# Performance work log

Hardware: AMD Instinct MI355X
Metric: run time of the kernel (lower is better)

## Reference

```python
import jax, jax.numpy as jnp
import numpy as np

N_NODES = 100000
N_EDGES = 1600000
DIM = 64
LN_EPS = 1e-5


def setup_inputs() -> dict:
    key = jax.random.key(0)
    ks = jax.random.split(key, 8)
    x = jax.random.normal(ks[0], (N_NODES, DIM), dtype=jnp.float32)
    edge_row = jax.random.randint(ks[1], (N_EDGES,), 0, N_NODES, dtype=jnp.int32)
    edge_col = jax.random.randint(ks[2], (N_EDGES,), 0, N_NODES, dtype=jnp.int32)
    edge_val = jax.random.uniform(ks[3], (N_EDGES,), dtype=jnp.float32)
    W = jax.random.normal(ks[4], (DIM, DIM), dtype=jnp.float32) * (1.0 / np.sqrt(DIM))
    b = jax.random.normal(ks[5], (DIM,), dtype=jnp.float32) * 0.01
    gamma = jnp.ones((DIM,), dtype=jnp.float32)
    beta = jnp.zeros((DIM,), dtype=jnp.float32)
    return {"x": x, "edge_row": edge_row, "edge_col": edge_col,
            "edge_val": edge_val, "W": W, "b": b, "gamma": gamma, "beta": beta}


def reference(x, edge_row, edge_col, edge_val, W, b, gamma, beta):
    # SpMM: out[r] += val * x[c] for each edge (r, c, val)  (= torch.sparse.mm(adj, x))
    msgs = edge_val[:, None] * x[edge_col]                      # [E, D]
    agg = jax.ops.segment_sum(msgs, edge_row, num_segments=x.shape[0])  # [N, D]
    # Linear
    h = agg @ W.T + b                                           # [N, D]
    # LayerNorm over last dim
    mu = jnp.mean(h, axis=-1, keepdims=True)
    var = jnp.mean(jnp.square(h - mu), axis=-1, keepdims=True)
    h = (h - mu) * jax.lax.rsqrt(var + LN_EPS) * gamma + beta
    # ReLU (dropout p=0.0 -> identity)
    return jax.nn.relu(h)
```

## Files before the change

### kernel.cpp

```cpp
#include <hip/hip_runtime.h>
#include <hip/hip_fp16.h>

#define DIM 64
#define RPB 128
#define NSCAT 512
#define MAXBUK 1024
#define ECAP 2432
#define CAP 384

typedef _Float16 half8_t __attribute__((ext_vector_type(8)));
typedef float f32x4_t __attribute__((ext_vector_type(4)));

__device__ __forceinline__ float readlane_f(float v, int l) {
  return __uint_as_float(__builtin_amdgcn_readlane(__float_as_uint(v), l));
}

__global__ __launch_bounds__(256) void scatter_kernel(
    const float* __restrict__ x, const int* __restrict__ erow,
    const int* __restrict__ ecol, const float* __restrict__ eval,
    float* __restrict__ agg, int E) {
  int t = blockIdx.x * 256 + threadIdx.x;
  int e = t >> 4;
  if (e >= E) return;
  int lid = t & 15;
  int r = erow[e];
  int c = ecol[e];
  float v = eval[e];
  const float4 xv =
      *reinterpret_cast<const float4*>(x + (size_t)c * DIM + lid * 4);
  float* dst = agg + (size_t)r * DIM + lid * 4;
  atomicAdd(dst + 0, v * xv.x);
  atomicAdd(dst + 1, v * xv.y);
  atomicAdd(dst + 2, v * xv.z);
  atomicAdd(dst + 3, v * xv.w);
}

__global__ __launch_bounds__(256) void fused_linear_ln_relu(
    const float* __restrict__ agg, const float* __restrict__ W,
    const float* __restrict__ bias, const float* __restrict__ gamma,
    const float* __restrict__ beta, float* __restrict__ out, int N) {
  __shared__ float Wt[64 * 65];
  for (int i = threadIdx.x; i < 64 * 64; i += 256) {
    int d = i >> 6, k = i & 63;
    Wt[k * 65 + d] = W[i];
  }
  __syncthreads();

  const int wave = threadIdx.x >> 6;
  const int lane = threadIdx.x & 63;
  const int node0 = blockIdx.x * 16 + wave * 4;

  float a0 = 0.f, a1 = 0.f, a2 = 0.f, a3 = 0.f;
  if (node0 + 0 < N) a0 = agg[(size_t)(node0 + 0) * DIM + lane];
  if (node0 + 1 < N) a1 = agg[(size_t)(node0 + 1) * DIM + lane];
  if (node0 + 2 < N) a2 = agg[(size_t)(node0 + 2) * DIM + lane];
  if (node0 + 3 < N) a3 = agg[(size_t)(node0 + 3) * DIM + lane];

  float acc0 = 0.f, acc1 = 0.f, acc2 = 0.f, acc3 = 0.f;
#pragma unroll
  for (int k = 0; k < 64; ++k) {
    float w = Wt[k * 65 + lane];
    acc0 = fmaf(readlane_f(a0, k), w, acc0);
    acc1 = fmaf(readlane_f(a1, k), w, acc1);
    acc2 = fmaf(readlane_f(a2, k), w, acc2);
    acc3 = fmaf(readlane_f(a3, k), w, acc3);
  }

  const float bv = bias[lane];
  const float gv = gamma[lane];
  const float btv = beta[lane];
  float accs[4] = {acc0, acc1, acc2, acc3};
#pragma unroll
  for (int j = 0; j < 4; ++j) {
    int node = node0 + j;
    if (node >= N) continue;
    float h = accs[j] + bv;
    float s1 = h, s2 = h * h;
#pragma unroll
    for (int off = 32; off; off >>= 1) {
      s1 += __shfl_xor(s1, off, 64);
      s2 += __shfl_xor(s2, off, 64);
    }
    float mu = s1 * (1.0f / 64.0f);
    float var = s2 * (1.0f / 64.0f) - mu * mu;
    float inv = rsqrtf(var + 1e-5f);
    float y = (h - mu) * inv * gv + btv;
    out[(size_t)node * DIM + lane] = fmaxf(y, 0.0f);
  }
}

__global__ __launch_bounds__(256) void scatter_reserve_and_cvt(
    const int* __restrict__ erow, const int* __restrict__ ecol,
    const float* __restrict__ eval, int* __restrict__ gcnt,
    uint2* __restrict__ binned, int E, int cpb, int NB,
    const float* __restrict__ x, __half* __restrict__ xh, int n4) {
  if (blockIdx.x >= NSCAT) {
    int i = (blockIdx.x - NSCAT) * 256 + threadIdx.x;
    if (i < n4) {
      float4 f = reinterpret_cast<const float4*>(x)[i];
      __half2 a = __floats2half2_rn(f.x, f.y);
      __half2 b = __floats2half2_rn(f.z, f.w);
      uint2 o;
      o.x = *reinterpret_cast<unsigned*>(&a);
      o.y = *reinterpret_cast<unsigned*>(&b);
      reinterpret_cast<uint2*>(xh)[i] = o;
    }
    return;
  }

  __shared__ int cnt_l[MAXBUK];
  __shared__ int cur_l[MAXBUK];

  const int tid = threadIdx.x;
  const int xcd = blockIdx.x & 7;
  const int base = blockIdx.x * cpb;
  const int end = min(E, base + cpb);

  for (int i = tid; i < NB; i += 256) cnt_l[i] = 0;
  __syncthreads();
  for (int e = base + tid; e < end; e += 256)
    atomicAdd(&cnt_l[erow[e] >> 7], 1);
  __syncthreads();
  for (int i = tid; i < NB; i += 256) {
    int c = cnt_l[i];
    cur_l[i] = c ? atomicAdd(&gcnt[xcd * NB + i], c) : 0;
  }
  __syncthreads();
  for (int e = base + tid; e < end; e += 256) {
    int r = erow[e];
    int b = r >> 7;
    uint2 p;
    p.x = ((unsigned)ecol[e] << 7) | (unsigned)(r & 127);
    p.y = __float_as_uint(eval[e]);
    int pos = atomicAdd(&cur_l[b], 1);
    if (pos < CAP)
      binned[(size_t)(xcd * NB + b) * CAP + pos] = p;
  }
}

template <typename XT>
__global__ __launch_bounds__(512) void fused_sort_gather_mfma_ln(
    const XT* __restrict__ xg, const uint2* __restrict__ binned,
    const int* __restrict__ gcnt, const float* __restrict__ W,
    const float* __restrict__ bias, const float* __restrict__ gamma,
    const float* __restrict__ beta, float* __restrict__ out, int N, int NB) {
  __shared__ uint2 ebuf[ECAP];
  __shared__ _Float16 A_lds[8][16 * 72];
  __shared__ int hist[RPB];
  __shared__ int rs_l[RPB + 1];
  __shared__ int cur[RPB];
  __shared__ int wsum2[2];

  const int tid = threadIdx.x;
  const int b = blockIdx.x;

  const int wave = tid >> 6;
  const int lane = tid & 63;
  const int gw = (tid >> 4) & 3;
  const int lid = tid & 15;

  if (tid < RPB) hist[tid] = 0;
  __syncthreads();
#pragma unroll 1
  for (int xcd = 0; xcd < 8; ++xcd) {
    const uint2* seg = binned + (size_t)(xcd * NB + b) * CAP;
    const int sc = min(gcnt[xcd * NB + b], CAP);
    for (int e = tid; e < sc; e += 512) atomicAdd(&hist[seg[e].x & 127], 1);
  }
  __syncthreads();
  {
    int v = (tid < RPB) ? hist[tid] : 0;
    int ps = v;
#pragma unroll
    for (int off = 1; off < 64; off <<= 1) {
      int nn = __shfl_up(ps, off, 64);
      if ((tid & 63) >= off) ps += nn;
    }
    if (tid == 63) wsum2[0] = ps;
    if (tid == 127) wsum2[1] = ps;
    __syncthreads();
    if (tid < RPB) {
      int ex = ps - v + (tid >= 64 ? wsum2[0] : 0);
      rs_l[tid] = min(ex, ECAP);
      cur[tid] = ex;
    }
    if (tid == 0) rs_l[RPB] = min(wsum2[0] + wsum2[1], ECAP);
    __syncthreads();
  }
#pragma unroll 1
  for (int xcd = 0; xcd < 8; ++xcd) {
    const uint2* seg = binned + (size_t)(xcd * NB + b) * CAP;
    const int sc = min(gcnt[xcd * NB + b], CAP);
    for (int e = tid; e < sc; e += 512) {
      uint2 p = seg[e];
      int pos = atomicAdd(&cur[p.x & 127], 1);
      if (pos < ECAP) ebuf[pos] = p;
    }
  }
  __syncthreads();

#pragma unroll 1
  for (int m = 0; m < 4; ++m) {
    const int lr = gw * 4 + m;
    const int rl = wave * 16 + lr;
    const int sl = rs_l[rl];
    const int el = max(rs_l[rl + 1], sl);
    float4 acc = make_float4(0.f, 0.f, 0.f, 0.f);
#pragma unroll 1
    for (int j = sl; j < el; j += 8) {
      uint2 p[8];
#pragma unroll
      for (int i = 0; i < 8; ++i) {
        int idx = j + i;
        idx = idx < el ? idx : el - 1;
        p[i] = ebuf[idx];
      }
      if constexpr (sizeof(XT) == 2) {
        uint2 xv[8];
#pragma unroll
        for (int i = 0; i < 8; ++i)
          xv[i] = *reinterpret_cast<const uint2*>(
              xg + (size_t)(p[i].x >> 7) * DIM + lid * 4);
#pragma unroll
        for (int i = 0; i < 8; ++i) {
          float v = (j + i < el) ? __uint_as_float(p[i].y) : 0.0f;
          float2 f01 = __half22float2(*reinterpret_cast<__half2*>(&xv[i].x));
          float2 f23 = __half22float2(*reinterpret_cast<__half2*>(&xv[i].y));
          acc.x = fmaf(v, f01.x, acc.x);
          acc.y = fmaf(v, f01.y, acc.y);
          acc.z = fmaf(v, f23.x, acc.z);
          acc.w = fmaf(v, f23.y, acc.w);
        }
      } else {
        float4 xv[8];
#pragma unroll
        for (int i = 0; i < 8; ++i)
          xv[i] = *reinterpret_cast<const float4*>(
              (const float*)xg + (size_t)(p[i].x >> 7) * DIM + lid * 4);
#pragma unroll
        for (int i = 0; i < 8; ++i) {
          float v = (j + i < el) ? __uint_as_float(p[i].y) : 0.0f;
          acc.x = fmaf(v, xv[i].x, acc.x);
          acc.y = fmaf(v, xv[i].y, acc.y);
          acc.z = fmaf(v, xv[i].z, acc.z);
          acc.w = fmaf(v, xv[i].w, acc.w);
        }
      }
    }
    __half2 lo = __floats2half2_rn(acc.x, acc.y);
    __half2 hi = __floats2half2_rn(acc.z, acc.w);
    uint2 pk;
    pk.x = *reinterpret_cast<unsigned*>(&lo);
    pk.y = *reinterpret_cast<unsigned*>(&hi);
    *reinterpret_cast<uint2*>(&A_lds[wave][lr * 72 + lid * 4]) = pk;
  }

  asm volatile("s_waitcnt lgkmcnt(0)" ::: "memory");
  __builtin_amdgcn_sched_barrier(0);

  const int dcol = lane & 15;
  const int kg = lane >> 4;

  half8_t bf[4][2];
#pragma unroll
  for (int t = 0; t < 4; ++t)
#pragma unroll
    for (int hh = 0; hh < 2; ++hh) {
      const float* wr = W + (dcol + 16 * t) * 64 + kg * 8 + 32 * hh;
      float4 w0 = *reinterpret_cast<const float4*>(wr);
      float4 w1 = *reinterpret_cast<const float4*>(wr + 4);
      half8_t hf;
      hf[0] = (_Float16)w0.x; hf[1] = (_Float16)w0.y;
      hf[2] = (_Float16)w0.z; hf[3] = (_Float16)w0.w;
      hf[4] = (_Float16)w1.x; hf[5] = (_Float16)w1.y;
      hf[6] = (_Float16)w1.z; hf[7] = (_Float16)w1.w;
      bf[t][hh] = hf;
    }

  half8_t af0 =
      *reinterpret_cast<const half8_t*>(&A_lds[wave][dcol * 72 + kg * 8]);
  half8_t af1 =
      *reinterpret_cast<const half8_t*>(&A_lds[wave][dcol * 72 + kg * 8 + 32]);

  f32x4_t dacc[4];
#pragma unroll
  for (int t = 0; t < 4; ++t) {
    f32x4_t z = {0.f, 0.f, 0.f, 0.f};
    z = __builtin_amdgcn_mfma_f32_16x16x32_f16(af0, bf[t][0], z, 0, 0, 0);
    z = __builtin_amdgcn_mfma_f32_16x16x32_f16(af1, bf[t][1], z, 0, 0, 0);
    dacc[t] = z;
  }

  const int q = lane >> 4;
  float bv[4], gv[4], btv[4];
#pragma unroll
  for (int t = 0; t < 4; ++t) {
    int d = dcol + 16 * t;
    bv[t] = bias[d];
    gv[t] = gamma[d];
    btv[t] = beta[d];
  }

#pragma unroll
  for (int j = 0; j < 4; ++j) {
    const int node = b * RPB + wave * 16 + q * 4 + j;
    float h0 = dacc[0][j] + bv[0];
    float h1 = dacc[1][j] + bv[1];
    float h2 = dacc[2][j] + bv[2];
    float h3 = dacc[3][j] + bv[3];
    float s1 = h0 + h1 + h2 + h3;
    float s2 = fmaf(h0, h0, fmaf(h1, h1, fmaf(h2, h2, h3 * h3)));
#pragma unroll
    for (int off = 1; off < 16; off <<= 1) {
      s1 += __shfl_xor(s1, off, 16);
      s2 += __shfl_xor(s2, off, 16);
    }
    float mu = s1 * (1.0f / 64.0f);
    float var = s2 * (1.0f / 64.0f) - mu * mu;
    float inv = rsqrtf(var + 1e-5f);
    if (node < N) {
      float* o = out + (size_t)node * DIM + dcol;
      o[0]  = fmaxf((h0 - mu) * inv * gv[0] + btv[0], 0.f);
      o[16] = fmaxf((h1 - mu) * inv * gv[1] + btv[1], 0.f);
      o[32] = fmaxf((h2 - mu) * inv * gv[2] + btv[2], 0.f);
      o[48] = fmaxf((h3 - mu) * inv * gv[3] + btv[3], 0.f);
    }
  }
}

extern "C" void kernel_launch(void* const* d_in, const int* in_sizes, int n_in,
                              void* d_out, int out_size, void* d_ws,
                              size_t ws_size, hipStream_t stream) {
  const float* x = (const float*)d_in[0];
  const int* erow = (const int*)d_in[1];
  const int* ecol = (const int*)d_in[2];
  const float* eval = (const float*)d_in[3];
  const float* W = (const float*)d_in[4];
  const float* bias = (const float*)d_in[5];
  const float* gamma = (const float*)d_in[6];
  const float* beta = (const float*)d_in[7];
  float* out = (float*)d_out;

  const int N = in_sizes[0] / DIM;
  const int E = in_sizes[1];

  const int NB = (N + RPB - 1) / RPB;
  const int cpb = (E + NSCAT - 1) / NSCAT;

  size_t gcnt_bytes = (size_t)8 * NB * sizeof(int);
  size_t binned_off = (gcnt_bytes + 15) & ~(size_t)15;
  size_t need_base = binned_off + (size_t)8 * NB * CAP * sizeof(uint2);
  size_t xh_off = (need_base + 15) & ~(size_t)15;
  size_t need_fp16 = xh_off + (size_t)N * DIM * sizeof(__half);

  if (ws_size >= need_base && NB <= MAXBUK) {
    int* gcnt = (int*)d_ws;
    uint2* binned = (uint2*)((char*)d_ws + binned_off);
    const bool use_fp16 = (ws_size >= need_fp16);
    __half* xh = (__half*)((char*)d_ws + xh_off);

    hipMemsetAsync(gcnt, 0, gcnt_bytes, stream);

    const int n4 = use_fp16 ? (N * DIM / 4) : 0;
    const int cvt_blocks = use_fp16 ? (n4 + 255) / 256 : 0;
    scatter_reserve_and_cvt<<<NSCAT + cvt_blocks, 256, 0, stream>>>(
        erow, ecol, eval, gcnt, binned, E, cpb, NB, x, xh, n4);
    if (use_fp16) {
      fused_sort_gather_mfma_ln<__half><<<NB, 512, 0, stream>>>(
          xh, binned, gcnt, W, bias, gamma, beta, out, N, NB);
    } else {
      fused_sort_gather_mfma_ln<float><<<NB, 512, 0, stream>>>(
          x, binned, gcnt, W, bias, gamma, beta, out, N, NB);
    }
  } else {
    const size_t agg_bytes = (size_t)N * DIM * sizeof(float);
    float* agg = (ws_size >= agg_bytes) ? (float*)d_ws : out;
    hipMemsetAsync(agg, 0, agg_bytes, stream);
    long long total = (long long)E * 16;
    int blocks = (int)((total + 255) / 256);
    scatter_kernel<<<blocks, 256, 0, stream>>>(x, erow, ecol, eval, agg, E);
    fused_linear_ln_relu<<<(N + 15) / 16, 256, 0, stream>>>(agg, W, bias,
                                                            gamma, beta, out, N);
  }
}
```

Before: 98.66 us.

## Cache binned edges in registers and widen fp16 gather to 16-byte loads

The binned-edge segments are now read once into registers (one entry per thread per XCD segment), used for both the histogram and the scatter passes, instead of being reloaded from global memory. The column index is pre-shifted when stored into LDS, so the gather loop no longer shifts it. For the fp16 path, each lane now loads 8 halves (16 bytes) per edge with 8 lanes per row and two rows per lane group, replacing 4-half loads with 16 lanes per row. This halves the number of load instructions and doubles the per-lane accumulator work. The register caching assumes each segment holds at most 512 entries, which holds because CAP is 384.

```diff
diff --git a/kernel.cpp b/kernel.cpp
--- a/kernel.cpp
+++ b/kernel.cpp
@@ -156,16 +156,22 @@
 
   const int wave = tid >> 6;
   const int lane = tid & 63;
-  const int gw = (tid >> 4) & 3;
-  const int lid = tid & 15;
-
+
+  uint2 myp[8];
+  bool myok[8];
   if (tid < RPB) hist[tid] = 0;
   __syncthreads();
-#pragma unroll 1
+#pragma unroll
   for (int xcd = 0; xcd < 8; ++xcd) {
     const uint2* seg = binned + (size_t)(xcd * NB + b) * CAP;
     const int sc = min(gcnt[xcd * NB + b], CAP);
-    for (int e = tid; e < sc; e += 512) atomicAdd(&hist[seg[e].x & 127], 1);
+    bool ok = tid < sc;
+    myok[xcd] = ok;
+    myp[xcd].x = 0; myp[xcd].y = 0;
+    if (ok) {
+      myp[xcd] = seg[tid];
+      atomicAdd(&hist[myp[xcd].x & 127], 1);
+    }
   }
   __syncthreads();
   {
@@ -187,56 +193,97 @@
     if (tid == 0) rs_l[RPB] = min(wsum2[0] + wsum2[1], ECAP);
     __syncthreads();
   }
+#pragma unroll
+  for (int xcd = 0; xcd < 8; ++xcd) {
+    if (myok[xcd]) {
+      uint2 p = myp[xcd];
+      int pos = atomicAdd(&cur[p.x & 127], 1);
+      if (pos < ECAP) {
+        uint2 q;
+        q.x = p.x >> 7;
+        q.y = p.y;
+        ebuf[pos] = q;
+      }
+    }
+  }
+  __syncthreads();
+
+  if constexpr (sizeof(XT) == 2) {
+    const int g8 = lane >> 3;
+    const int l8 = lane & 7;
 #pragma unroll 1
-  for (int xcd = 0; xcd < 8; ++xcd) {
-    const uint2* seg = binned + (size_t)(xcd * NB + b) * CAP;
-    const int sc = min(gcnt[xcd * NB + b], CAP);
-    for (int e = tid; e < sc; e += 512) {
-      uint2 p = seg[e];
-      int pos = atomicAdd(&cur[p.x & 127], 1);
-      if (pos < ECAP) ebuf[pos] = p;
-    }
-  }
-  __syncthreads();
-
+    for (int m = 0; m < 2; ++m) {
+      const int lr = g8 * 2 + m;
+      const int rl = wave * 16 + lr;
+      const int sl = rs_l[rl];
+      const int el = max(rs_l[rl + 1], sl);
+      float a[8] = {0.f, 0.f, 0.f, 0.f, 0.f, 0.f, 0.f, 0.f};
 #pragma unroll 1
-  for (int m = 0; m < 4; ++m) {
-    const int lr = gw * 4 + m;
-    const int rl = wave * 16 + lr;
-    const int sl = rs_l[rl];
-    const int el = max(rs_l[rl + 1], sl);
-    float4 acc = make_float4(0.f, 0.f, 0.f, 0.f);
-#pragma unroll 1
-    for (int j = sl; j < el; j += 8) {
-      uint2 p[8];
-#pragma unroll
-      for (int i = 0; i < 8; ++i) {
-        int idx = j + i;
-        idx = idx < el ? idx : el - 1;
-        p[i] = ebuf[idx];
-      }
-      if constexpr (sizeof(XT) == 2) {
-        uint2 xv[8];
+      for (int j = sl; j < el; j += 8) {
+        uint2 p[8];
+#pragma unroll
+        for (int i = 0; i < 8; ++i) {
+          int idx = j + i;
+          idx = idx < el ? idx : el - 1;
+          p[i] = ebuf[idx];
+        }
+        uint4 xv[8];
 #pragma unroll
         for (int i = 0; i < 8; ++i)
-          xv[i] = *reinterpret_cast<const uint2*>(
-              xg + (size_t)(p[i].x >> 7) * DIM + lid * 4);
+          xv[i] = *reinterpret_cast<const uint4*>(
+              xg + (size_t)p[i].x * DIM + l8 * 8);
 #pragma unroll
         for (int i = 0; i < 8; ++i) {
           float v = (j + i < el) ? __uint_as_float(p[i].y) : 0.0f;
-          float2 f01 = __half22float2(*reinterpret_cast<__half2*>(&xv[i].x));
-          float2 f23 = __half22float2(*reinterpret_cast<__half2*>(&xv[i].y));
-          acc.x = fmaf(v, f01.x, acc.x);
-          acc.y = fmaf(v, f01.y, acc.y);
-          acc.z = fmaf(v, f23.x, acc.z);
-          acc.w = fmaf(v, f23.y, acc.w);
+          float2 f0 = __half22float2(*reinterpret_cast<__half2*>(&xv[i].x));
+          float2 f1 = __half22float2(*reinterpret_cast<__half2*>(&xv[i].y));
+          float2 f2 = __half22float2(*reinterpret_cast<__half2*>(&xv[i].z));
+          float2 f3 = __half22float2(*reinterpret_cast<__half2*>(&xv[i].w));
+          a[0] = fmaf(v, f0.x, a[0]);
+          a[1] = fmaf(v, f0.y, a[1]);
+          a[2] = fmaf(v, f1.x, a[2]);
+          a[3] = fmaf(v, f1.y, a[3]);
+          a[4] = fmaf(v, f2.x, a[4]);
+          a[5] = fmaf(v, f2.y, a[5]);
+          a[6] = fmaf(v, f3.x, a[6]);
+          a[7] = fmaf(v, f3.y, a[7]);
         }
-      } else {
+      }
+      __half2 h0 = __floats2half2_rn(a[0], a[1]);
+      __half2 h1 = __floats2half2_rn(a[2], a[3]);
+      __half2 h2 = __floats2half2_rn(a[4], a[5]);
+      __half2 h3 = __floats2half2_rn(a[6], a[7]);
+      uint4 pk;
+      pk.x = *reinterpret_cast<unsigned*>(&h0);
+      pk.y = *reinterpret_cast<unsigned*>(&h1);
+      pk.z = *reinterpret_cast<unsigned*>(&h2);
+      pk.w = *reinterpret_cast<unsigned*>(&h3);
+      *reinterpret_cast<uint4*>(&A_lds[wave][lr * 72 + l8 * 8]) = pk;
+    }
+  } else {
+    const int gw = (tid >> 4) & 3;
+    const int lid = tid & 15;
+#pragma unroll 1
+    for (int m = 0; m < 4; ++m) {
+      const int lr = gw * 4 + m;
+      const int rl = wave * 16 + lr;
+      const int sl = rs_l[rl];
+      const int el = max(rs_l[rl + 1], sl);
+      float4 acc = make_float4(0.f, 0.f, 0.f, 0.f);
+#pragma unroll 1
+      for (int j = sl; j < el; j += 8) {
+        uint2 p[8];
+#pragma unroll
+        for (int i = 0; i < 8; ++i) {
+          int idx = j + i;
+          idx = idx < el ? idx : el - 1;
+          p[i] = ebuf[idx];
+        }
         float4 xv[8];
 #pragma unroll
         for (int i = 0; i < 8; ++i)
           xv[i] = *reinterpret_cast<const float4*>(
-              (const float*)xg + (size_t)(p[i].x >> 7) * DIM + lid * 4);
+              (const float*)xg + (size_t)p[i].x * DIM + lid * 4);
 #pragma unroll
         for (int i = 0; i < 8; ++i) {
           float v = (j + i < el) ? __uint_as_float(p[i].y) : 0.0f;
@@ -246,13 +293,13 @@
           acc.w = fmaf(v, xv[i].w, acc.w);
         }
       }
-    }
-    __half2 lo = __floats2half2_rn(acc.x, acc.y);
-    __half2 hi = __floats2half2_rn(acc.z, acc.w);
-    uint2 pk;
-    pk.x = *reinterpret_cast<unsigned*>(&lo);
-    pk.y = *reinterpret_cast<unsigned*>(&hi);
-    *reinterpret_cast<uint2*>(&A_lds[wave][lr * 72 + lid * 4]) = pk;
+      __half2 lo = __floats2half2_rn(acc.x, acc.y);
+      __half2 hi = __floats2half2_rn(acc.z, acc.w);
+      uint2 pk;
+      pk.x = *reinterpret_cast<unsigned*>(&lo);
+      pk.y = *reinterpret_cast<unsigned*>(&hi);
+      *reinterpret_cast<uint2*>(&A_lds[wave][lr * 72 + lid * 4]) = pk;
+    }
   }
 
   asm volatile("s_waitcnt lgkmcnt(0)" ::: "memory");
```

New measurement: 103.7 us. 5.1% more time.
